# Kernel optimization log

Measured on AMD Instinct MI355X. Metric: run time of the kernel, lower is better.

Reference implementation:

```python
import jax, jax.numpy as jnp
import numpy as np

TAYLOR_ORDER = 16      # Taylor terms after scaling (||A_s|| <= 0.5 -> machine precision)
MAX_SQUARINGS = 16     # fixed upper bound on squaring steps (jit-friendly)


def batched_expm(A):
    """Vectorized scaling-and-squaring matrix exponential for A of shape [..., n, n].

    Replaces the original per-item torch.linalg.matrix_exp Python loop with one
    fused batched computation (same math: exp(Q*t)).
    """
    n = A.shape[-1]
    I = jnp.eye(n, dtype=A.dtype)
    # per-matrix infinity norm [...,]
    nrm = jnp.max(jnp.sum(jnp.abs(A), axis=-1), axis=-1)
    # number of squarings so that scaled norm <= 0.5
    s = jnp.clip(jnp.ceil(jnp.log2(jnp.maximum(nrm, 1e-30) / 0.5)), 0.0, float(MAX_SQUARINGS))
    As = A * jnp.exp2(-s)[..., None, None]
    # Taylor series: P = I + As + As^2/2! + ...
    P = jnp.broadcast_to(I, A.shape)
    term = P
    for k in range(1, TAYLOR_ORDER + 1):
        term = jnp.matmul(term, As) / k
        P = P + term
    # undo scaling: square s times (data-dependent count via masked squaring)
    s_b = s[..., None, None]
    for i in range(MAX_SQUARINGS):
        P = jnp.where(s_b > i, jnp.matmul(P, P), P)
    return P


def setup_inputs() -> dict:
    key = jax.random.key(0)
    k1, k2 = jax.random.split(key)
    rate_matrix = jax.random.normal(k1, (64, 32768, 4, 4), dtype=jnp.float32)
    time = jax.random.uniform(k2, (64,), dtype=jnp.float32)
    return {"rate_matrix": rate_matrix, "time": time}


def reference(rate_matrix, time):
    # Qt = rate_matrix[i, j] * time[i], batched over (batch, seq_len)
    Qt = rate_matrix * time[:, None, None, None]
    return batched_expm(Qt)  # [B, S, 4, 4] transition probability matrices
```

## Files before the change

### kernel.cpp

```cpp
#include <hip/hip_runtime.h>
#include <math.h>


typedef float v2f __attribute__((ext_vector_type(2)));

__device__ __forceinline__ void mm4(const v2f (&Am)[4][2],
                                    const v2f (&Bm)[4][2],
                                    v2f (&Cm)[4][2])
{
#pragma unroll
    for (int i = 0; i < 4; ++i) {
        const float a0 = Am[i][0][0], a1 = Am[i][0][1];
        const float a2 = Am[i][1][0], a3 = Am[i][1][1];
#pragma unroll
        for (int p = 0; p < 2; ++p) {
            v2f acc = Cm[i][p];
            acc += a0 * Bm[0][p];
            acc += a1 * Bm[1][p];
            acc += a2 * Bm[2][p];
            acc += a3 * Bm[3][p];
            Cm[i][p] = acc;
        }
    }
}

__global__ void __launch_bounds__(256) expm4_kernel(
    const float* __restrict__ A,
    const float* __restrict__ tvec,
    float* __restrict__ out,
    int M, int S)
{
    const int m = blockIdx.x * 256 + threadIdx.x;
    if (m >= M) return;

    const float t = tvec[m / S];

    const float4* Ap = reinterpret_cast<const float4*>(A) + (size_t)m * 4;
    float4 r[4];
#pragma unroll
    for (int i = 0; i < 4; ++i) r[i] = Ap[i];

    float nrm = 0.0f;
#pragma unroll
    for (int i = 0; i < 4; ++i) {
        float rs = fabsf(r[i].x) + fabsf(r[i].y) + fabsf(r[i].z) + fabsf(r[i].w);
        nrm = fmaxf(nrm, rs);
    }
    float sf = ceilf(log2f(fmaxf(t * nrm, 1e-30f) * 2.0f));
    sf = fminf(fmaxf(sf, 0.0f), 16.0f);
    const int   si = (int)sf;
    const float c  = t * ldexpf(1.0f, -si);

    v2f X[4][2];
#pragma unroll
    for (int i = 0; i < 4; ++i) {
        X[i][0][0] = r[i].x * c;  X[i][0][1] = r[i].y * c;
        X[i][1][0] = r[i].z * c;  X[i][1][1] = r[i].w * c;
    }

    v2f X2[4][2] = {};  mm4(X,  X, X2);
    v2f X3[4][2] = {};  mm4(X2, X, X3);

    constexpr float c2 = 1.f/2.f,   c3 = 1.f/6.f,    c4 = 1.f/24.f;
    constexpr float c5 = 1.f/120.f, c6 = 1.f/720.f,  c7 = 1.f/5040.f;
    constexpr float c8 = 1.f/40320.f;

    v2f B2[4][2];
#pragma unroll
    for (int i = 0; i < 4; ++i) {
#pragma unroll
        for (int p = 0; p < 2; ++p) B2[i][p] = c7 * X[i][p] + c8 * X2[i][p];
    }
    B2[0][0][0] += c6; B2[1][0][1] += c6; B2[2][1][0] += c6; B2[3][1][1] += c6;

    v2f T1[4][2];
#pragma unroll
    for (int i = 0; i < 4; ++i) {
#pragma unroll
        for (int p = 0; p < 2; ++p) T1[i][p] = c4 * X[i][p] + c5 * X2[i][p];
    }
    T1[0][0][0] += c3; T1[1][0][1] += c3; T1[2][1][0] += c3; T1[3][1][1] += c3;
    mm4(X3, B2, T1);

    v2f P[4][2];
#pragma unroll
    for (int i = 0; i < 4; ++i) {
#pragma unroll
        for (int p = 0; p < 2; ++p) P[i][p] = X[i][p] + c2 * X2[i][p];
    }
    P[0][0][0] += 1.f; P[1][0][1] += 1.f; P[2][1][0] += 1.f; P[3][1][1] += 1.f;
    mm4(X3, T1, P);

    for (int it = 0; it < si; ++it) {
        v2f Q[4][2] = {};
        mm4(P, P, Q);
#pragma unroll
        for (int i = 0; i < 4; ++i) {
            P[i][0] = Q[i][0];
            P[i][1] = Q[i][1];
        }
    }

    float4* Op = reinterpret_cast<float4*>(out) + (size_t)m * 4;
#pragma unroll
    for (int i = 0; i < 4; ++i) {
        float4 v;
        v.x = P[i][0][0]; v.y = P[i][0][1];
        v.z = P[i][1][0]; v.w = P[i][1][1];
        Op[i] = v;
    }
}

extern "C" void kernel_launch(void* const* d_in, const int* in_sizes, int n_in,
                              void* d_out, int out_size, void* d_ws, size_t ws_size,
                              hipStream_t stream) {
    const float* A    = (const float*)d_in[0];
    const float* tvec = (const float*)d_in[1];
    float* out        = (float*)d_out;

    const int B = in_sizes[1];
    const int M = in_sizes[0] / 16;
    const int S = M / B;

    const int threads = 256;
    const int blocks  = (M + threads - 1) / threads;
    expm4_kernel<<<blocks, threads, 0, stream>>>(A, tvec, out, M, S);
}
```

Before: 232.9 us.

## Process four matrices per thread with interleaved stages and nontemporal stores

Each thread now handles four consecutive 4x4 matrices, interleaving their independent Taylor stages to expose ILP. Output is written with nontemporal stores, and launch bounds request two blocks per CU. The cost is higher register pressure, a quarter as many threads, and strided per-thread memory access (each thread reads a 256-byte contiguous chunk), which may hurt coalescing.

```diff
diff --git a/kernel.cpp b/kernel.cpp
--- a/kernel.cpp
+++ b/kernel.cpp
@@ -3,6 +3,9 @@
 
 
 typedef float v2f __attribute__((ext_vector_type(2)));
+typedef float v4f __attribute__((ext_vector_type(4)));
+
+constexpr int K = 4;
 
 __device__ __forceinline__ void mm4(const v2f (&Am)[4][2],
                                     const v2f (&Bm)[4][2],
@@ -24,90 +27,125 @@
     }
 }
 
-__global__ void __launch_bounds__(256) expm4_kernel(
+template <int KK>
+__device__ __forceinline__ void expm_run(const float* __restrict__ A,
+                                         const float* __restrict__ tvec,
+                                         float* __restrict__ out,
+                                         int m0, int S)
+{
+    const int q = m0 / S;
+    const int r = m0 - q * S;
+
+    const v4f* Ap = reinterpret_cast<const v4f*>(A) + (size_t)m0 * 4;
+    v4f L[KK][4];
+#pragma unroll
+    for (int k = 0; k < KK; ++k)
+#pragma unroll
+        for (int i = 0; i < 4; ++i)
+            L[k][i] = Ap[4 * k + i];
+
+    constexpr float c2 = 1.f/2.f,   c3 = 1.f/6.f,    c4 = 1.f/24.f;
+    constexpr float c5 = 1.f/120.f, c6 = 1.f/720.f,  c7 = 1.f/5040.f;
+    constexpr float c8 = 1.f/40320.f;
+
+    v2f X[KK][4][2], X2[KK][4][2], X3[KK][4][2], T1[KK][4][2], P[KK][4][2];
+    int si[KK];
+
+#pragma unroll
+    for (int k = 0; k < KK; ++k) {
+        const float t = tvec[q + ((r + k) >= S ? 1 : 0)];
+        float nrm = 0.0f;
+#pragma unroll
+        for (int i = 0; i < 4; ++i) {
+            float rs = fabsf(L[k][i][0]) + fabsf(L[k][i][1])
+                     + fabsf(L[k][i][2]) + fabsf(L[k][i][3]);
+            nrm = fmaxf(nrm, rs);
+        }
+        float sf = ceilf(log2f(fmaxf(t * nrm, 1e-30f) * 2.0f));
+        sf = fminf(fmaxf(sf, 0.0f), 16.0f);
+        si[k] = (int)sf;
+        const float c = t * ldexpf(1.0f, -si[k]);
+#pragma unroll
+        for (int i = 0; i < 4; ++i) {
+            X[k][i][0] = v2f{L[k][i][0], L[k][i][1]} * c;
+            X[k][i][1] = v2f{L[k][i][2], L[k][i][3]} * c;
+        }
+    }
+
+#pragma unroll
+    for (int k = 0; k < KK; ++k) {
+#pragma unroll
+        for (int i = 0; i < 4; ++i) { X2[k][i][0] = v2f{0.f,0.f}; X2[k][i][1] = v2f{0.f,0.f}; }
+        mm4(X[k], X[k], X2[k]);
+    }
+#pragma unroll
+    for (int k = 0; k < KK; ++k) {
+#pragma unroll
+        for (int i = 0; i < 4; ++i) { X3[k][i][0] = v2f{0.f,0.f}; X3[k][i][1] = v2f{0.f,0.f}; }
+        mm4(X2[k], X[k], X3[k]);
+    }
+
+#pragma unroll
+    for (int k = 0; k < KK; ++k) {
+        v2f B2[4][2];
+#pragma unroll
+        for (int i = 0; i < 4; ++i)
+#pragma unroll
+            for (int p = 0; p < 2; ++p) B2[i][p] = c7 * X[k][i][p] + c8 * X2[k][i][p];
+        B2[0][0][0] += c6; B2[1][0][1] += c6; B2[2][1][0] += c6; B2[3][1][1] += c6;
+
+#pragma unroll
+        for (int i = 0; i < 4; ++i)
+#pragma unroll
+            for (int p = 0; p < 2; ++p) T1[k][i][p] = c4 * X[k][i][p] + c5 * X2[k][i][p];
+        T1[k][0][0][0] += c3; T1[k][1][0][1] += c3; T1[k][2][1][0] += c3; T1[k][3][1][1] += c3;
+        mm4(X3[k], B2, T1[k]);
+    }
+#pragma unroll
+    for (int k = 0; k < KK; ++k) {
+#pragma unroll
+        for (int i = 0; i < 4; ++i)
+#pragma unroll
+            for (int p = 0; p < 2; ++p) P[k][i][p] = X[k][i][p] + c2 * X2[k][i][p];
+        P[k][0][0][0] += 1.f; P[k][1][0][1] += 1.f; P[k][2][1][0] += 1.f; P[k][3][1][1] += 1.f;
+        mm4(X3[k], T1[k], P[k]);
+    }
+
+#pragma unroll
+    for (int k = 0; k < KK; ++k) {
+        for (int it = 0; it < si[k]; ++it) {
+            v2f Q[4][2] = {};
+            mm4(P[k], P[k], Q);
+#pragma unroll
+            for (int i = 0; i < 4; ++i) { P[k][i][0] = Q[i][0]; P[k][i][1] = Q[i][1]; }
+        }
+    }
+
+    v4f* Og = reinterpret_cast<v4f*>(out) + (size_t)m0 * 4;
+#pragma unroll
+    for (int k = 0; k < KK; ++k)
+#pragma unroll
+        for (int i = 0; i < 4; ++i) {
+            v4f v = {P[k][i][0][0], P[k][i][0][1],
+                     P[k][i][1][0], P[k][i][1][1]};
+            __builtin_nontemporal_store(v, Og + 4 * k + i);
+        }
+}
+
+__global__ void __launch_bounds__(256, 2) expm4_kernel(
     const float* __restrict__ A,
     const float* __restrict__ tvec,
     float* __restrict__ out,
     int M, int S)
 {
-    const int m = blockIdx.x * 256 + threadIdx.x;
-    if (m >= M) return;
+    const int tid = blockIdx.x * 256 + threadIdx.x;
+    int m0 = tid * K;
+    if (m0 >= M) return;
 
-    const float t = tvec[m / S];
-
-    const float4* Ap = reinterpret_cast<const float4*>(A) + (size_t)m * 4;
-    float4 r[4];
-#pragma unroll
-    for (int i = 0; i < 4; ++i) r[i] = Ap[i];
-
-    float nrm = 0.0f;
-#pragma unroll
-    for (int i = 0; i < 4; ++i) {
-        float rs = fabsf(r[i].x) + fabsf(r[i].y) + fabsf(r[i].z) + fabsf(r[i].w);
-        nrm = fmaxf(nrm, rs);
-    }
-    float sf = ceilf(log2f(fmaxf(t * nrm, 1e-30f) * 2.0f));
-    sf = fminf(fmaxf(sf, 0.0f), 16.0f);
-    const int   si = (int)sf;
-    const float c  = t * ldexpf(1.0f, -si);
-
-    v2f X[4][2];
-#pragma unroll
-    for (int i = 0; i < 4; ++i) {
-        X[i][0][0] = r[i].x * c;  X[i][0][1] = r[i].y * c;
-        X[i][1][0] = r[i].z * c;  X[i][1][1] = r[i].w * c;
-    }
-
-    v2f X2[4][2] = {};  mm4(X,  X, X2);
-    v2f X3[4][2] = {};  mm4(X2, X, X3);
-
-    constexpr float c2 = 1.f/2.f,   c3 = 1.f/6.f,    c4 = 1.f/24.f;
-    constexpr float c5 = 1.f/120.f, c6 = 1.f/720.f,  c7 = 1.f/5040.f;
-    constexpr float c8 = 1.f/40320.f;
-
-    v2f B2[4][2];
-#pragma unroll
-    for (int i = 0; i < 4; ++i) {
-#pragma unroll
-        for (int p = 0; p < 2; ++p) B2[i][p] = c7 * X[i][p] + c8 * X2[i][p];
-    }
-    B2[0][0][0] += c6; B2[1][0][1] += c6; B2[2][1][0] += c6; B2[3][1][1] += c6;
-
-    v2f T1[4][2];
-#pragma unroll
-    for (int i = 0; i < 4; ++i) {
-#pragma unroll
-        for (int p = 0; p < 2; ++p) T1[i][p] = c4 * X[i][p] + c5 * X2[i][p];
-    }
-    T1[0][0][0] += c3; T1[1][0][1] += c3; T1[2][1][0] += c3; T1[3][1][1] += c3;
-    mm4(X3, B2, T1);
-
-    v2f P[4][2];
-#pragma unroll
-    for (int i = 0; i < 4; ++i) {
-#pragma unroll
-        for (int p = 0; p < 2; ++p) P[i][p] = X[i][p] + c2 * X2[i][p];
-    }
-    P[0][0][0] += 1.f; P[1][0][1] += 1.f; P[2][1][0] += 1.f; P[3][1][1] += 1.f;
-    mm4(X3, T1, P);
-
-    for (int it = 0; it < si; ++it) {
-        v2f Q[4][2] = {};
-        mm4(P, P, Q);
-#pragma unroll
-        for (int i = 0; i < 4; ++i) {
-            P[i][0] = Q[i][0];
-            P[i][1] = Q[i][1];
-        }
-    }
-
-    float4* Op = reinterpret_cast<float4*>(out) + (size_t)m * 4;
-#pragma unroll
-    for (int i = 0; i < 4; ++i) {
-        float4 v;
-        v.x = P[i][0][0]; v.y = P[i][0][1];
-        v.z = P[i][1][0]; v.w = P[i][1][1];
-        Op[i] = v;
+    if (m0 + K <= M) {
+        expm_run<K>(A, tvec, out, m0, S);
+    } else {
+        for (; m0 < M; ++m0) expm_run<1>(A, tvec, out, m0, S);
     }
 }
 
@@ -123,6 +161,7 @@
     const int S = M / B;
 
     const int threads = 256;
-    const int blocks  = (M + threads - 1) / threads;
+    const int matPerBlock = threads * K;
+    const int blocks = (M + matPerBlock - 1) / matPerBlock;
     expm4_kernel<<<blocks, threads, 0, stream>>>(A, tvec, out, M, S);
 }
```

New measurement: 448.9 us. 92.7% more time.
